# Kernel tuning notes

Measured on AMD Instinct MI355X. Metric: run time of the kernel, lower is better.

The kernel has to match this reference:

```python
import jax, jax.numpy as jnp
import numpy as np
import math

B, CIN, COUT, H, W, K, SDIM = 8, 512, 512, 64, 64, 3, 512
EPS = 1e-8
NEG_SLOPE = 0.2
SCALE = math.sqrt(2.0)


def setup_inputs() -> dict:
    key = jax.random.key(0)
    ks = jax.random.split(key, 7)
    x = jax.random.normal(ks[0], (B, CIN, H, W), jnp.float32)
    style = jax.random.normal(ks[1], (B, SDIM), jnp.float32)
    noise = jax.random.normal(ks[2], (B, 1, H, W), jnp.float32)
    # kernel stored as (kh, kw, Cin, Cout) like keras Conv2D
    fan_in = K * K * CIN
    kernel = jax.random.normal(ks[3], (K, K, CIN, COUT), jnp.float32) / math.sqrt(fan_in)
    style_scale = jax.random.normal(ks[4], (SDIM, COUT), jnp.float32) * 0.02
    bias = jax.random.normal(ks[5], (COUT,), jnp.float32) * 0.01
    noise_weight = jax.random.normal(ks[6], (1,), jnp.float32) * 0.1
    return {"x": x, "style": style, "noise": noise, "kernel": kernel,
            "style_scale": style_scale, "bias": bias, "noise_weight": noise_weight}


def _styled_conv(x, style, noise, kernel, style_scale, bias, noise_weight):
    b = x.shape[0]
    # --- modulation ---
    s = style @ style_scale                              # [B, Cout]
    w = kernel[None] * (s[:, None, None, None, :] + 1.0)  # [B, kh, kw, Cin, Cout]
    # --- demodulation ---
    d = jax.lax.rsqrt(jnp.sum(jnp.square(w), axis=(1, 2, 3)) + EPS)  # [B, Cout]
    w = w * d[:, None, None, None, :]
    # --- per-sample conv via batch-as-groups trick ---
    # weights -> OIHW with O = B*Cout, groups = B
    w_oihw = jnp.transpose(w, (0, 4, 3, 1, 2)).reshape(b * COUT, CIN, K, K)
    x_g = x.reshape(1, b * CIN, H, W)
    out = jax.lax.conv_general_dilated(
        x_g, w_oihw, window_strides=(1, 1), padding="SAME",
        feature_group_count=b,
        dimension_numbers=("NCHW", "OIHW", "NCHW"))
    out = out.reshape(b, COUT, H, W)
    # --- noise injection ---
    out = out + noise_weight[0] * noise                  # noise broadcasts over channels
    # --- fused bias + leaky relu * sqrt(2) ---
    out = jax.nn.leaky_relu(out + bias[None, :, None, None], NEG_SLOPE) * SCALE
    return out


def reference(x, style, noise, kernel, style_scale, bias, noise_weight):
    return _styled_conv(x, style, noise, kernel, style_scale, bias, noise_weight)
```

## Files before the change

kernel.cpp:

```cpp
#include <hip/hip_runtime.h>

#define B_     8
#define CIN_   512
#define COUT_  512
#define HW_    64
#define SDIM_  512
#define NPIX   4096
#define KTOT   4608
#define PADW   66

typedef __attribute__((ext_vector_type(4))) float f32x4;
typedef __attribute__((ext_vector_type(8))) short bf16x8;
typedef __attribute__((ext_vector_type(8))) unsigned short u16x8;

__device__ __forceinline__ float bf2f(unsigned short b) {
    unsigned int u = ((unsigned int)b) << 16;
    return __builtin_bit_cast(float, u);
}
__device__ __forceinline__ unsigned short f2bf(float f) {
    unsigned int u = __builtin_bit_cast(unsigned int, f);
    return (unsigned short)((u + 0x7fffu + ((u >> 16) & 1u)) >> 16);
}
__device__ __forceinline__ float ldin(const void* p, size_t i, int isbf) {
    return isbf ? bf2f(((const unsigned short*)p)[i]) : ((const float*)p)[i];
}

#define GLD16(g, l) __builtin_amdgcn_global_load_lds( \
    (__attribute__((address_space(1))) void*)(g),     \
    (__attribute__((address_space(3))) void*)(l), 16, 0, 0)

__global__ void detect_dtype(const unsigned int* __restrict__ style_u32,
                             int* __restrict__ flag) {
    int t = threadIdx.x;
    unsigned int w = style_u32[t * 4];
    int e = (w >> 7) & 0xFF;
    int isbf = (e >= 110 && e <= 140) ? 1 : 0;
    __shared__ int cnt;
    if (t == 0) cnt = 0;
    __syncthreads();
    atomicAdd(&cnt, isbf);
    __syncthreads();
    if (t == 0) *flag = (cnt >= 128) ? 1 : 0;
}

__global__ void halo_zero(unsigned short* __restrict__ xtp) {
    int idx = blockIdx.x;
    int b = blockIdx.y;
    int y, x;
    if (idx < 66)       { y = 0;  x = idx; }
    else if (idx < 132) { y = 65; x = idx - 66; }
    else if (idx < 196) { x = 0;  y = idx - 131; }
    else                { x = 65; y = idx - 195; }
    unsigned int* dst = (unsigned int*)(xtp + (((size_t)b * PADW + y) * PADW + x) * CIN_);
    dst[threadIdx.x] = 0;
}

__global__ void wt_transpose(const void* __restrict__ kin,
                             unsigned short* __restrict__ wt,
                             const int* __restrict__ flag) {
    __shared__ __align__(16) unsigned short tile[64][72];
    int isbf = *flag;
    int t = threadIdx.x;
    int co0 = blockIdx.x * 64;
    int k0  = blockIdx.y * 64;
    int r = t >> 2, c16 = (t & 3) << 4;
    if (isbf) {
        const unsigned short* src = (const unsigned short*)kin + (size_t)(k0 + r) * COUT_ + co0 + c16;
        *(u16x8*)&tile[r][c16]     = *(const u16x8*)src;
        *(u16x8*)&tile[r][c16 + 8] = *(const u16x8*)(src + 8);
    } else {
        const float* src = (const float*)kin + (size_t)(k0 + r) * COUT_ + co0 + c16;
#pragma unroll
        for (int q = 0; q < 4; ++q) {
            f32x4 v = *(const f32x4*)(src + q * 4);
#pragma unroll
            for (int j = 0; j < 4; ++j) tile[r][c16 + q * 4 + j] = f2bf(v[j]);
        }
    }
    __syncthreads();
    int c = t >> 2, r16 = (t & 3) << 4;
    u16x8 w0, w1;
#pragma unroll
    for (int j = 0; j < 8; ++j) { w0[j] = tile[r16 + j][c]; w1[j] = tile[r16 + 8 + j][c]; }
    unsigned short* dst = wt + (size_t)(co0 + c) * KTOT + k0 + r16;
    *(u16x8*)dst       = w0;
    *(u16x8*)(dst + 8) = w1;
}

__global__ void xpose(const void* __restrict__ x,
                      unsigned short* __restrict__ xtp,
                      const int* __restrict__ flag) {
    __shared__ __align__(16) unsigned short tile[64][72];
    int isbf = *flag;
    int t = threadIdx.x;
    int cit = blockIdx.x;
    int y   = blockIdx.y;
    int b   = blockIdx.z;
    int ci_l = t >> 2, xo = (t & 3) << 4;
    size_t srcoff = (((size_t)(b * CIN_ + cit * 64 + ci_l)) * HW_ + y) * HW_ + xo;
    if (isbf) {
        const unsigned short* src = (const unsigned short*)x + srcoff;
        *(u16x8*)&tile[ci_l][xo]     = *(const u16x8*)src;
        *(u16x8*)&tile[ci_l][xo + 8] = *(const u16x8*)(src + 8);
    } else {
        const float* src = (const float*)x + srcoff;
#pragma unroll
        for (int q = 0; q < 4; ++q) {
            f32x4 v = *(const f32x4*)(src + q * 4);
#pragma unroll
            for (int j = 0; j < 4; ++j) tile[ci_l][xo + q * 4 + j] = f2bf(v[j]);
        }
    }
    __syncthreads();
    int xl = t >> 2, cio = (t & 3) << 4;
    u16x8 w0, w1;
#pragma unroll
    for (int j = 0; j < 8; ++j) { w0[j] = tile[cio + j][xl]; w1[j] = tile[cio + 8 + j][xl]; }
    unsigned short* dst =
        xtp + (((size_t)b * PADW + (y + 1)) * PADW + (xl + 1)) * CIN_ + cit * 64 + cio;
    *(u16x8*)dst       = w0;
    *(u16x8*)(dst + 8) = w1;
}

__global__ void mod_kernel(const void* __restrict__ style,
                           const void* __restrict__ sscale,
                           const unsigned short* __restrict__ wt,
                           float* __restrict__ mmod,
                           const int* __restrict__ flag) {
    int isbf = *flag;
    int co = blockIdx.x, t = threadIdx.x;
    int lane = t & 63, wid = t >> 6;
    float k2 = 0.f;
    const unsigned short* wr = wt + (size_t)co * KTOT;
    for (int k = t; k < KTOT; k += 256) { float v = bf2f(wr[k]); k2 += v * v; }
    float sb[B_];
#pragma unroll
    for (int b = 0; b < B_; ++b) sb[b] = 0.f;
    for (int sd = t; sd < SDIM_; sd += 256) {
        float ss = ldin(sscale, (size_t)sd * COUT_ + co, isbf);
#pragma unroll
        for (int b = 0; b < B_; ++b) sb[b] += ldin(style, b * SDIM_ + sd, isbf) * ss;
    }
    __shared__ float red[4][9];
    float vals[9];
    vals[0] = k2;
#pragma unroll
    for (int b = 0; b < B_; ++b) vals[1 + b] = sb[b];
#pragma unroll
    for (int q = 0; q < 9; ++q) {
        float v = vals[q];
        for (int off = 32; off; off >>= 1) v += __shfl_down(v, off);
        if (lane == 0) red[wid][q] = v;
    }
    __syncthreads();
    if (t < B_) {
        int b = t;
        float k2t = red[0][0] + red[1][0] + red[2][0] + red[3][0];
        float s   = red[0][1 + b] + red[1][1 + b] + red[2][1 + b] + red[3][1 + b];
        float sp1 = s + 1.f;
        mmod[b * COUT_ + co] = sp1 * rsqrtf(sp1 * sp1 * k2t + 1e-8f);
    }
}

__global__ __launch_bounds__(512, 2) void conv_gemm(
    const unsigned short* __restrict__ wt,
    const unsigned short* __restrict__ xtp,
    const float* __restrict__ mmod,
    const void* __restrict__ noise,
    const void* __restrict__ bias,
    const void* __restrict__ nwp,
    void* __restrict__ out,
    const int* __restrict__ flag) {
    __shared__ __align__(1024) unsigned short Asm[2][256 * 64];
    __shared__ __align__(1024) unsigned short Bsm[2][256 * 64];
    int isbf = *flag;
    int tid = threadIdx.x;
    int lane = tid & 63, wid = tid >> 6;
    int lr = lane & 15, hi = lane >> 4;
    int wm = wid >> 2, wn = wid & 3;

    int bid = blockIdx.x;
    int swz = (bid & 7) * 32 + (bid >> 3);
    int gy = swz >> 7;
    int nb = swz & 127;
    int b  = nb >> 4;
    int nt = nb & 15;
    int pl0 = nt << 8;
    int h0  = pl0 >> 6;
    int co0 = gy << 8;

    const unsigned short* xb = xtp + (size_t)b * (PADW * PADW * CIN_);

    f32x4 acc[8][4];
#pragma unroll
    for (int i = 0; i < 8; ++i)
#pragma unroll
        for (int j = 0; j < 4; ++j) acc[i][j] = (f32x4){0.f, 0.f, 0.f, 0.f};

    int rsub = lane >> 3;
    int ce_src = ((lane & 7) ^ rsub) << 3;
    int swzr = (lane & 7) << 3;

    auto stageA = [&](int tt, int pp, int q) {
        const unsigned short* srcA =
            wt + (size_t)(co0 + (q << 6) + (wid << 3) + rsub) * KTOT + (tt << 6) + ce_src;
        GLD16(srcA, (char*)&Asm[pp][0] + (q << 13) + (wid << 10));
    };
    auto stageB = [&](int tt, int pp, int q) {
        int khw = tt >> 3;
        int kh = (khw >= 6) ? 2 : ((khw >= 3) ? 1 : 0);
        int kw = khw - kh * 3;
        int ci0 = (tt & 7) << 6;
        int wc = ((wid << 3) + rsub) & 63;
        const unsigned short* srcB =
            xb + ((size_t)(h0 + q + kh) * PADW + (wc + kw)) * CIN_ + ci0 + ce_src;
        GLD16(srcB, (char*)&Bsm[pp][0] + (q << 13) + (wid << 10));
    };

#pragma unroll
    for (int q = 0; q < 4; ++q) { stageA(0, 0, q); stageB(0, 0, q); }
    asm volatile("s_waitcnt vmcnt(0)" ::: "memory");
    __builtin_amdgcn_s_barrier();
    asm volatile("" ::: "memory");

    for (int t = 0; t < 72; ++t) {
        int p = t & 1, pn = p ^ 1;
        const unsigned short* As = &Asm[p][0];
        const unsigned short* Bs = &Bsm[p][0];

        if (t < 71) {
#pragma unroll
            for (int q = 0; q < 4; ++q) { stageA(t + 1, pn, q); stageB(t + 1, pn, q); }
        }

        bf16x8 a0[4], bk0[4];
#pragma unroll
        for (int i = 0; i < 4; ++i)
            a0[i] = *(const bf16x8*)&As[(((wm << 7) + (i << 4) + lr) << 6) + ((hi << 3) ^ swzr)];
#pragma unroll
        for (int i = 0; i < 4; ++i)
            bk0[i] = *(const bf16x8*)&Bs[(((wn << 6) + (i << 4) + lr) << 6) + ((hi << 3) ^ swzr)];
        __builtin_amdgcn_s_setprio(1);
#pragma unroll
        for (int mf = 0; mf < 4; ++mf)
#pragma unroll
            for (int nf = 0; nf < 4; ++nf)
                acc[mf][nf] = __builtin_amdgcn_mfma_f32_16x16x32_bf16(a0[mf], bk0[nf], acc[mf][nf], 0, 0, 0);
        __builtin_amdgcn_s_setprio(0);

        bf16x8 a1[4];
#pragma unroll
        for (int i = 0; i < 4; ++i)
            a1[i] = *(const bf16x8*)&As[(((wm << 7) + ((i + 4) << 4) + lr) << 6) + ((hi << 3) ^ swzr)];
        __builtin_amdgcn_s_setprio(1);
#pragma unroll
        for (int mf = 0; mf < 4; ++mf)
#pragma unroll
            for (int nf = 0; nf < 4; ++nf)
                acc[mf + 4][nf] = __builtin_amdgcn_mfma_f32_16x16x32_bf16(a1[mf], bk0[nf], acc[mf + 4][nf], 0, 0, 0);
        __builtin_amdgcn_s_setprio(0);

        bf16x8 a2[4], bk1[4];
#pragma unroll
        for (int i = 0; i < 4; ++i)
            a2[i] = *(const bf16x8*)&As[(((wm << 7) + (i << 4) + lr) << 6) + ((32 + (hi << 3)) ^ swzr)];
#pragma unroll
        for (int i = 0; i < 4; ++i)
            bk1[i] = *(const bf16x8*)&Bs[(((wn << 6) + (i << 4) + lr) << 6) + ((32 + (hi << 3)) ^ swzr)];
        __builtin_amdgcn_s_setprio(1);
#pragma unroll
        for (int mf = 0; mf < 4; ++mf)
#pragma unroll
            for (int nf = 0; nf < 4; ++nf)
                acc[mf][nf] = __builtin_amdgcn_mfma_f32_16x16x32_bf16(a2[mf], bk1[nf], acc[mf][nf], 0, 0, 0);
        __builtin_amdgcn_s_setprio(0);

        bf16x8 a3[4];
#pragma unroll
        for (int i = 0; i < 4; ++i)
            a3[i] = *(const bf16x8*)&As[(((wm << 7) + ((i + 4) << 4) + lr) << 6) + ((32 + (hi << 3)) ^ swzr)];
        __builtin_amdgcn_s_setprio(1);
#pragma unroll
        for (int mf = 0; mf < 4; ++mf)
#pragma unroll
            for (int nf = 0; nf < 4; ++nf)
                acc[mf + 4][nf] = __builtin_amdgcn_mfma_f32_16x16x32_bf16(a3[mf], bk1[nf], acc[mf + 4][nf], 0, 0, 0);
        __builtin_amdgcn_s_setprio(0);

        asm volatile("s_waitcnt lgkmcnt(0)" ::: "memory");
        if (t < 71) asm volatile("s_waitcnt vmcnt(0)" ::: "memory");
        __builtin_amdgcn_s_barrier();
        asm volatile("" ::: "memory");
    }

    float nw = ldin(nwp, 0, isbf);
    unsigned short* out16 = (unsigned short*)out;
    float* outf = (float*)out;
#pragma unroll
    for (int mf = 0; mf < 8; ++mf) {
        int cobase = co0 + (wm << 7) + (mf << 4) + (hi << 2);
        f32x4 mv = *(const f32x4*)&mmod[b * COUT_ + cobase];
        float bb[4];
#pragma unroll
        for (int r = 0; r < 4; ++r) bb[r] = ldin(bias, cobase + r, isbf);
#pragma unroll
        for (int nf = 0; nf < 4; ++nf) {
            int pix = pl0 + (wn << 6) + (nf << 4) + lr;
            float nv = nw * ldin(noise, b * NPIX + pix, isbf);
#pragma unroll
            for (int r = 0; r < 4; ++r) {
                float v = acc[mf][nf][r] * mv[r] + nv + bb[r];
                v = (v < 0.f ? v * 0.2f : v) * 1.41421356237f;
                size_t oidx = ((size_t)(b * COUT_ + cobase + r)) * NPIX + pix;
                if (isbf) out16[oidx] = f2bf(v);
                else      outf[oidx]  = v;
            }
        }
    }
}

extern "C" void kernel_launch(void* const* d_in, const int* in_sizes, int n_in,
                              void* d_out, int out_size, void* d_ws, size_t ws_size,
                              hipStream_t stream) {
    const void* x      = d_in[0];
    const void* style  = d_in[1];
    const void* noise  = d_in[2];
    const void* kin    = d_in[3];
    const void* sscale = d_in[4];
    const void* bias   = d_in[5];
    const void* nwp    = d_in[6];

    char* ws = (char*)d_ws;
    int* flag = (int*)ws;
    const size_t xtp_off  = 256;
    const size_t xtp_bytes = (size_t)B_ * PADW * PADW * CIN_ * 2;
    const size_t wt_bytes  = (size_t)COUT_ * KTOT * 2;
    unsigned short* xtp = (unsigned short*)(ws + xtp_off);
    unsigned short* wtr = (unsigned short*)(ws + xtp_off + xtp_bytes);
    float* mmod         = (float*)(ws + xtp_off + xtp_bytes + wt_bytes);

    detect_dtype<<<1, 256, 0, stream>>>((const unsigned int*)style, flag);
    halo_zero<<<dim3(260, 8), 256, 0, stream>>>(xtp);
    wt_transpose<<<dim3(8, 72), 256, 0, stream>>>(kin, wtr, flag);
    xpose<<<dim3(8, 64, 8), 256, 0, stream>>>(x, xtp, flag);
    mod_kernel<<<512, 256, 0, stream>>>(style, sscale, wtr, mmod, flag);
    conv_gemm<<<256, 512, 0, stream>>>(wtr, xtp, mmod, noise, bias, nwp, d_out, flag);
}
```

Measured before the change: 202.8 us.

## Restructure GEMM main loop into 8-phase ping-pong schedule with interleaved staging

Replaces the simple double-buffered K loop, which issued all global-to-LDS loads for the next tile and then waited for all of them, with a two-tile unrolled loop of eight phases. Each phase issues a quarter of the next tile's A/B loads, reads a subset of fragments from LDS, and runs 16 MFMAs under barriers, with partial vmcnt/lgkmcnt waits. The goal is to overlap global loads, LDS reads and MFMA work more finely and keep loads in flight across iterations. In exchange it adds many more barriers per iteration and relies on hand-tuned waitcnt values, which could stall or race if any of those counts are wrong.

```diff
diff --git a/kernel.cpp b/kernel.cpp
--- a/kernel.cpp
+++ b/kernel.cpp
@@ -216,81 +216,155 @@
             xb + ((size_t)(h0 + q + kh) * PADW + (wc + kw)) * CIN_ + ci0 + ce_src;
         GLD16(srcB, (char*)&Bsm[pp][0] + (q << 13) + (wid << 10));
     };
+    auto rdA = [&](const unsigned short* Bp, int mi, int kk) -> bf16x8 {
+        return *(const bf16x8*)&Bp[(((wm << 7) + (mi << 4) + lr) << 6) +
+                                   (((kk << 5) + (hi << 3)) ^ swzr)];
+    };
+    auto rdB = [&](const unsigned short* Bp, int ni, int kk) -> bf16x8 {
+        return *(const bf16x8*)&Bp[(((wn << 6) + (ni << 4) + lr) << 6) +
+                                   (((kk << 5) + (hi << 3)) ^ swzr)];
+    };
+
+#define PH_SYNC12  asm volatile("s_waitcnt lgkmcnt(8)" ::: "memory");
+#define PH_TOP     __builtin_amdgcn_s_barrier(); \
+                   asm volatile("s_waitcnt lgkmcnt(0)" ::: "memory"); \
+                   __builtin_amdgcn_s_setprio(1);
+#define PH_END     __builtin_amdgcn_s_setprio(0);
+#define PH_BAR     __builtin_amdgcn_s_barrier(); asm volatile("" ::: "memory");
 
 #pragma unroll
     for (int q = 0; q < 4; ++q) { stageA(0, 0, q); stageB(0, 0, q); }
-    asm volatile("s_waitcnt vmcnt(0)" ::: "memory");
+    stageB(1, 1, 0); stageB(1, 1, 1); stageA(1, 1, 0); stageA(1, 1, 1);
+    asm volatile("s_waitcnt vmcnt(4)" ::: "memory");
     __builtin_amdgcn_s_barrier();
     asm volatile("" ::: "memory");
 
-    for (int t = 0; t < 72; ++t) {
-        int p = t & 1, pn = p ^ 1;
-        const unsigned short* As = &Asm[p][0];
-        const unsigned short* Bs = &Bsm[p][0];
-
-        if (t < 71) {
-#pragma unroll
-            for (int q = 0; q < 4; ++q) { stageA(t + 1, pn, q); stageB(t + 1, pn, q); }
-        }
-
-        bf16x8 a0[4], bk0[4];
-#pragma unroll
-        for (int i = 0; i < 4; ++i)
-            a0[i] = *(const bf16x8*)&As[(((wm << 7) + (i << 4) + lr) << 6) + ((hi << 3) ^ swzr)];
-#pragma unroll
-        for (int i = 0; i < 4; ++i)
-            bk0[i] = *(const bf16x8*)&Bs[(((wn << 6) + (i << 4) + lr) << 6) + ((hi << 3) ^ swzr)];
-        __builtin_amdgcn_s_setprio(1);
-#pragma unroll
-        for (int mf = 0; mf < 4; ++mf)
-#pragma unroll
-            for (int nf = 0; nf < 4; ++nf)
-                acc[mf][nf] = __builtin_amdgcn_mfma_f32_16x16x32_bf16(a0[mf], bk0[nf], acc[mf][nf], 0, 0, 0);
-        __builtin_amdgcn_s_setprio(0);
-
-        bf16x8 a1[4];
-#pragma unroll
-        for (int i = 0; i < 4; ++i)
-            a1[i] = *(const bf16x8*)&As[(((wm << 7) + ((i + 4) << 4) + lr) << 6) + ((hi << 3) ^ swzr)];
-        __builtin_amdgcn_s_setprio(1);
-#pragma unroll
-        for (int mf = 0; mf < 4; ++mf)
-#pragma unroll
-            for (int nf = 0; nf < 4; ++nf)
-                acc[mf + 4][nf] = __builtin_amdgcn_mfma_f32_16x16x32_bf16(a1[mf], bk0[nf], acc[mf + 4][nf], 0, 0, 0);
-        __builtin_amdgcn_s_setprio(0);
-
-        bf16x8 a2[4], bk1[4];
-#pragma unroll
-        for (int i = 0; i < 4; ++i)
-            a2[i] = *(const bf16x8*)&As[(((wm << 7) + (i << 4) + lr) << 6) + ((32 + (hi << 3)) ^ swzr)];
-#pragma unroll
-        for (int i = 0; i < 4; ++i)
-            bk1[i] = *(const bf16x8*)&Bs[(((wn << 6) + (i << 4) + lr) << 6) + ((32 + (hi << 3)) ^ swzr)];
-        __builtin_amdgcn_s_setprio(1);
-#pragma unroll
-        for (int mf = 0; mf < 4; ++mf)
-#pragma unroll
-            for (int nf = 0; nf < 4; ++nf)
-                acc[mf][nf] = __builtin_amdgcn_mfma_f32_16x16x32_bf16(a2[mf], bk1[nf], acc[mf][nf], 0, 0, 0);
-        __builtin_amdgcn_s_setprio(0);
-
-        bf16x8 a3[4];
-#pragma unroll
-        for (int i = 0; i < 4; ++i)
-            a3[i] = *(const bf16x8*)&As[(((wm << 7) + ((i + 4) << 4) + lr) << 6) + ((32 + (hi << 3)) ^ swzr)];
-        __builtin_amdgcn_s_setprio(1);
-#pragma unroll
-        for (int mf = 0; mf < 4; ++mf)
-#pragma unroll
-            for (int nf = 0; nf < 4; ++nf)
-                acc[mf + 4][nf] = __builtin_amdgcn_mfma_f32_16x16x32_bf16(a3[mf], bk1[nf], acc[mf + 4][nf], 0, 0, 0);
-        __builtin_amdgcn_s_setprio(0);
-
-        asm volatile("s_waitcnt lgkmcnt(0)" ::: "memory");
-        if (t < 71) asm volatile("s_waitcnt vmcnt(0)" ::: "memory");
-        __builtin_amdgcn_s_barrier();
-        asm volatile("" ::: "memory");
+    for (int i = 0; i < 36; ++i) {
+        int tY = 2 * i + 1;
+        bool sg = (i < 35);
+        const unsigned short* Xa = &Asm[0][0];
+        const unsigned short* Xb = &Bsm[0][0];
+        const unsigned short* Ya = &Asm[1][0];
+        const unsigned short* Yb = &Bsm[1][0];
+        bf16x8 aL[4][2], aH[4][2], bL[2][2], bR[2][2];
+
+#pragma unroll
+        for (int mi = 0; mi < 4; ++mi) { aL[mi][0] = rdA(Xa, mi, 0); aL[mi][1] = rdA(Xa, mi, 1); }
+#pragma unroll
+        for (int ni = 0; ni < 2; ++ni) { bL[ni][0] = rdB(Xb, ni, 0); bL[ni][1] = rdB(Xb, ni, 1); }
+        stageA(tY, 1, 2); stageA(tY, 1, 3);
+        PH_SYNC12
+        PH_TOP
+#pragma unroll
+        for (int mi = 0; mi < 4; ++mi)
+#pragma unroll
+            for (int ni = 0; ni < 2; ++ni) {
+                acc[mi][ni] = __builtin_amdgcn_mfma_f32_16x16x32_bf16(aL[mi][0], bL[ni][0], acc[mi][ni], 0, 0, 0);
+                acc[mi][ni] = __builtin_amdgcn_mfma_f32_16x16x32_bf16(aL[mi][1], bL[ni][1], acc[mi][ni], 0, 0, 0);
+            }
+        PH_END
+        PH_BAR
+
+#pragma unroll
+        for (int ni = 0; ni < 2; ++ni) { bR[ni][0] = rdB(Xb, ni + 2, 0); bR[ni][1] = rdB(Xb, ni + 2, 1); }
+        stageB(tY, 1, 2); stageB(tY, 1, 3);
+        PH_TOP
+#pragma unroll
+        for (int mi = 0; mi < 4; ++mi)
+#pragma unroll
+            for (int ni = 0; ni < 2; ++ni) {
+                acc[mi][ni + 2] = __builtin_amdgcn_mfma_f32_16x16x32_bf16(aL[mi][0], bR[ni][0], acc[mi][ni + 2], 0, 0, 0);
+                acc[mi][ni + 2] = __builtin_amdgcn_mfma_f32_16x16x32_bf16(aL[mi][1], bR[ni][1], acc[mi][ni + 2], 0, 0, 0);
+            }
+        PH_END
+        PH_BAR
+
+#pragma unroll
+        for (int mi = 0; mi < 4; ++mi) { aH[mi][0] = rdA(Xa, mi + 4, 0); aH[mi][1] = rdA(Xa, mi + 4, 1); }
+        if (sg) { stageB(2 * i + 2, 0, 0); stageB(2 * i + 2, 0, 1); }
+        PH_TOP
+#pragma unroll
+        for (int mi = 0; mi < 4; ++mi)
+#pragma unroll
+            for (int ni = 0; ni < 2; ++ni) {
+                acc[mi + 4][ni] = __builtin_amdgcn_mfma_f32_16x16x32_bf16(aH[mi][0], bL[ni][0], acc[mi + 4][ni], 0, 0, 0);
+                acc[mi + 4][ni] = __builtin_amdgcn_mfma_f32_16x16x32_bf16(aH[mi][1], bL[ni][1], acc[mi + 4][ni], 0, 0, 0);
+            }
+        PH_END
+        PH_BAR
+
+        if (sg) { stageA(2 * i + 2, 0, 0); stageA(2 * i + 2, 0, 1); }
+        PH_TOP
+#pragma unroll
+        for (int mi = 0; mi < 4; ++mi)
+#pragma unroll
+            for (int ni = 0; ni < 2; ++ni) {
+                acc[mi + 4][ni + 2] = __builtin_amdgcn_mfma_f32_16x16x32_bf16(aH[mi][0], bR[ni][0], acc[mi + 4][ni + 2], 0, 0, 0);
+                acc[mi + 4][ni + 2] = __builtin_amdgcn_mfma_f32_16x16x32_bf16(aH[mi][1], bR[ni][1], acc[mi + 4][ni + 2], 0, 0, 0);
+            }
+        PH_END
+        if (sg) asm volatile("s_waitcnt vmcnt(4)" ::: "memory");
+        else    asm volatile("s_waitcnt vmcnt(0)" ::: "memory");
+        PH_BAR
+
+#pragma unroll
+        for (int mi = 0; mi < 4; ++mi) { aL[mi][0] = rdA(Ya, mi, 0); aL[mi][1] = rdA(Ya, mi, 1); }
+#pragma unroll
+        for (int ni = 0; ni < 2; ++ni) { bL[ni][0] = rdB(Yb, ni, 0); bL[ni][1] = rdB(Yb, ni, 1); }
+        if (sg) { stageB(2 * i + 2, 0, 2); stageB(2 * i + 2, 0, 3); }
+        PH_SYNC12
+        PH_TOP
+#pragma unroll
+        for (int mi = 0; mi < 4; ++mi)
+#pragma unroll
+            for (int ni = 0; ni < 2; ++ni) {
+                acc[mi][ni] = __builtin_amdgcn_mfma_f32_16x16x32_bf16(aL[mi][0], bL[ni][0], acc[mi][ni], 0, 0, 0);
+                acc[mi][ni] = __builtin_amdgcn_mfma_f32_16x16x32_bf16(aL[mi][1], bL[ni][1], acc[mi][ni], 0, 0, 0);
+            }
+        PH_END
+        PH_BAR
+
+#pragma unroll
+        for (int ni = 0; ni < 2; ++ni) { bR[ni][0] = rdB(Yb, ni + 2, 0); bR[ni][1] = rdB(Yb, ni + 2, 1); }
+        if (sg) { stageA(2 * i + 2, 0, 2); stageA(2 * i + 2, 0, 3); }
+        PH_TOP
+#pragma unroll
+        for (int mi = 0; mi < 4; ++mi)
+#pragma unroll
+            for (int ni = 0; ni < 2; ++ni) {
+                acc[mi][ni + 2] = __builtin_amdgcn_mfma_f32_16x16x32_bf16(aL[mi][0], bR[ni][0], acc[mi][ni + 2], 0, 0, 0);
+                acc[mi][ni + 2] = __builtin_amdgcn_mfma_f32_16x16x32_bf16(aL[mi][1], bR[ni][1], acc[mi][ni + 2], 0, 0, 0);
+            }
+        PH_END
+        PH_BAR
+
+#pragma unroll
+        for (int mi = 0; mi < 4; ++mi) { aH[mi][0] = rdA(Ya, mi + 4, 0); aH[mi][1] = rdA(Ya, mi + 4, 1); }
+        if (sg) { stageB(2 * i + 3, 1, 0); stageB(2 * i + 3, 1, 1); }
+        PH_TOP
+#pragma unroll
+        for (int mi = 0; mi < 4; ++mi)
+#pragma unroll
+            for (int ni = 0; ni < 2; ++ni) {
+                acc[mi + 4][ni] = __builtin_amdgcn_mfma_f32_16x16x32_bf16(aH[mi][0], bL[ni][0], acc[mi + 4][ni], 0, 0, 0);
+                acc[mi + 4][ni] = __builtin_amdgcn_mfma_f32_16x16x32_bf16(aH[mi][1], bL[ni][1], acc[mi + 4][ni], 0, 0, 0);
+            }
+        PH_END
+        PH_BAR
+
+        if (sg) { stageA(2 * i + 3, 1, 0); stageA(2 * i + 3, 1, 1); }
+        PH_TOP
+#pragma unroll
+        for (int mi = 0; mi < 4; ++mi)
+#pragma unroll
+            for (int ni = 0; ni < 2; ++ni) {
+                acc[mi + 4][ni + 2] = __builtin_amdgcn_mfma_f32_16x16x32_bf16(aH[mi][0], bR[ni][0], acc[mi + 4][ni + 2], 0, 0, 0);
+                acc[mi + 4][ni + 2] = __builtin_amdgcn_mfma_f32_16x16x32_bf16(aH[mi][1], bR[ni][1], acc[mi + 4][ni + 2], 0, 0, 0);
+            }
+        PH_END
+        if (sg) asm volatile("s_waitcnt vmcnt(4)" ::: "memory");
+        else    asm volatile("s_waitcnt vmcnt(0)" ::: "memory");
+        PH_BAR
     }
 
     float nw = ldin(nwp, 0, isbf);
```

New measurement: 188.2 us. -7.2%, faster.

## Stage input halo window in LDS once per channel tile, reuse across 3x3 taps

Applied to the files above, without the earlier changes.

The padded activation buffer is re-laid out as [b][cin/64][66][66][64] so each 64-channel slab is contiguous. The conv GEMM now loads a 6x72x64 halo window into LDS once per channel tile and reads all nine kernel taps from it with shifted, swizzled offsets, instead of reloading an im2col B tile from global memory at every K step. The K loop order becomes channel-tile outer and tap inner, and the weight staging offsets change to match. The cost is an extra barrier and a non-overlapped window load at each channel-tile boundary, plus possible LDS bank conflicts from the tap-dependent swizzle.

```diff
diff --git a/kernel.cpp b/kernel.cpp
--- a/kernel.cpp
+++ b/kernel.cpp
@@ -43,7 +43,7 @@
     if (t == 0) *flag = (cnt >= 128) ? 1 : 0;
 }
 
-__global__ void halo_zero(unsigned short* __restrict__ xtp) {
+__global__ void halo_zero(unsigned int* __restrict__ xtp2u) {
     int idx = blockIdx.x;
     int b = blockIdx.y;
     int y, x;
@@ -51,8 +51,10 @@
     else if (idx < 132) { y = 65; x = idx - 66; }
     else if (idx < 196) { x = 0;  y = idx - 131; }
     else                { x = 65; y = idx - 195; }
-    unsigned int* dst = (unsigned int*)(xtp + (((size_t)b * PADW + y) * PADW + x) * CIN_);
-    dst[threadIdx.x] = 0;
+    int t = threadIdx.x;
+    int cit = t >> 5, j = t & 31;
+    size_t u32i = ((((size_t)(b * 8 + cit) * 66 + y) * 66 + x) << 5) + j;
+    xtp2u[u32i] = 0;
 }
 
 __global__ void wt_transpose(const void* __restrict__ kin,
@@ -88,7 +90,7 @@
 }
 
 __global__ void xpose(const void* __restrict__ x,
-                      unsigned short* __restrict__ xtp,
+                      unsigned short* __restrict__ xtp2,
                       const int* __restrict__ flag) {
     __shared__ __align__(16) unsigned short tile[64][72];
     int isbf = *flag;
@@ -117,7 +119,7 @@
 #pragma unroll
     for (int j = 0; j < 8; ++j) { w0[j] = tile[cio + j][xl]; w1[j] = tile[cio + 8 + j][xl]; }
     unsigned short* dst =
-        xtp + (((size_t)b * PADW + (y + 1)) * PADW + (xl + 1)) * CIN_ + cit * 64 + cio;
+        xtp2 + ((((size_t)(b * 8 + cit) * 66 + (y + 1)) * 66 + (xl + 1)) << 6) + cio;
     *(u16x8*)dst       = w0;
     *(u16x8*)(dst + 8) = w1;
 }
@@ -164,7 +166,7 @@
 
 __global__ __launch_bounds__(512, 2) void conv_gemm(
     const unsigned short* __restrict__ wt,
-    const unsigned short* __restrict__ xtp,
+    const unsigned short* __restrict__ xtp2,
     const float* __restrict__ mmod,
     const void* __restrict__ noise,
     const void* __restrict__ bias,
@@ -172,7 +174,7 @@
     void* __restrict__ out,
     const int* __restrict__ flag) {
     __shared__ __align__(1024) unsigned short Asm[2][256 * 64];
-    __shared__ __align__(1024) unsigned short Bsm[2][256 * 64];
+    __shared__ __align__(1024) unsigned short Win[6 * 72 * 64];
     int isbf = *flag;
     int tid = threadIdx.x;
     int lane = tid & 63, wid = tid >> 6;
@@ -189,8 +191,6 @@
     int h0  = pl0 >> 6;
     int co0 = gy << 8;
 
-    const unsigned short* xb = xtp + (size_t)b * (PADW * PADW * CIN_);
-
     f32x4 acc[8][4];
 #pragma unroll
     for (int i = 0; i < 8; ++i)
@@ -200,97 +200,117 @@
     int rsub = lane >> 3;
     int ce_src = ((lane & 7) ^ rsub) << 3;
     int swzr = (lane & 7) << 3;
-
-    auto stageA = [&](int tt, int pp, int q) {
+    int wsrc = (rsub << 6) + (((lane & 7) ^ (rsub & 7)) << 3);
+    int l7 = lane & 7;
+    int px[4];
+#pragma unroll
+    for (int ni = 0; ni < 4; ++ni) px[ni] = ((ni << 4) + lr) << 6;
+
+    auto stageA = [&](int koff, int pp, int q) {
         const unsigned short* srcA =
-            wt + (size_t)(co0 + (q << 6) + (wid << 3) + rsub) * KTOT + (tt << 6) + ce_src;
+            wt + (size_t)(co0 + (q << 6) + (wid << 3) + rsub) * KTOT + koff + ce_src;
         GLD16(srcA, (char*)&Asm[pp][0] + (q << 13) + (wid << 10));
     };
-    auto stageB = [&](int tt, int pp, int q) {
-        int khw = tt >> 3;
-        int kh = (khw >= 6) ? 2 : ((khw >= 3) ? 1 : 0);
-        int kw = khw - kh * 3;
-        int ci0 = (tt & 7) << 6;
-        int wc = ((wid << 3) + rsub) & 63;
-        const unsigned short* srcB =
-            xb + ((size_t)(h0 + q + kh) * PADW + (wc + kw)) * CIN_ + ci0 + ce_src;
-        GLD16(srcB, (char*)&Bsm[pp][0] + (q << 13) + (wid << 10));
+    auto stage_win = [&](int cit) {
+        size_t base = ((size_t)(b * 8 + cit) * 66 + h0) * (66 * 64);
+        for (int idx = wid; idx < 54; idx += 8) {
+            int r = idx / 9, g = idx - r * 9;
+            const unsigned short* src = xtp2 + base + (size_t)r * (66 * 64) + (g << 9) + wsrc;
+            GLD16(src, (char*)Win + r * 9216 + (g << 10));
+        }
     };
 
-#pragma unroll
-    for (int q = 0; q < 4; ++q) { stageA(0, 0, q); stageB(0, 0, q); }
+    stage_win(0);
+#pragma unroll
+    for (int q = 0; q < 4; ++q) stageA(0, 0, q);
     asm volatile("s_waitcnt vmcnt(0)" ::: "memory");
     __builtin_amdgcn_s_barrier();
     asm volatile("" ::: "memory");
 
-    for (int t = 0; t < 72; ++t) {
-        int p = t & 1, pn = p ^ 1;
-        const unsigned short* As = &Asm[p][0];
-        const unsigned short* Bs = &Bsm[p][0];
-
-        if (t < 71) {
-#pragma unroll
-            for (int q = 0; q < 4; ++q) { stageA(t + 1, pn, q); stageB(t + 1, pn, q); }
-        }
-
-        bf16x8 a0[4], bk0[4];
-#pragma unroll
-        for (int i = 0; i < 4; ++i)
-            a0[i] = *(const bf16x8*)&As[(((wm << 7) + (i << 4) + lr) << 6) + ((hi << 3) ^ swzr)];
-#pragma unroll
-        for (int i = 0; i < 4; ++i)
-            bk0[i] = *(const bf16x8*)&Bs[(((wn << 6) + (i << 4) + lr) << 6) + ((hi << 3) ^ swzr)];
-        __builtin_amdgcn_s_setprio(1);
-#pragma unroll
-        for (int mf = 0; mf < 4; ++mf)
-#pragma unroll
-            for (int nf = 0; nf < 4; ++nf)
-                acc[mf][nf] = __builtin_amdgcn_mfma_f32_16x16x32_bf16(a0[mf], bk0[nf], acc[mf][nf], 0, 0, 0);
-        __builtin_amdgcn_s_setprio(0);
-
-        bf16x8 a1[4];
-#pragma unroll
-        for (int i = 0; i < 4; ++i)
-            a1[i] = *(const bf16x8*)&As[(((wm << 7) + ((i + 4) << 4) + lr) << 6) + ((hi << 3) ^ swzr)];
-        __builtin_amdgcn_s_setprio(1);
-#pragma unroll
-        for (int mf = 0; mf < 4; ++mf)
-#pragma unroll
-            for (int nf = 0; nf < 4; ++nf)
-                acc[mf + 4][nf] = __builtin_amdgcn_mfma_f32_16x16x32_bf16(a1[mf], bk0[nf], acc[mf + 4][nf], 0, 0, 0);
-        __builtin_amdgcn_s_setprio(0);
-
-        bf16x8 a2[4], bk1[4];
-#pragma unroll
-        for (int i = 0; i < 4; ++i)
-            a2[i] = *(const bf16x8*)&As[(((wm << 7) + (i << 4) + lr) << 6) + ((32 + (hi << 3)) ^ swzr)];
-#pragma unroll
-        for (int i = 0; i < 4; ++i)
-            bk1[i] = *(const bf16x8*)&Bs[(((wn << 6) + (i << 4) + lr) << 6) + ((32 + (hi << 3)) ^ swzr)];
-        __builtin_amdgcn_s_setprio(1);
-#pragma unroll
-        for (int mf = 0; mf < 4; ++mf)
-#pragma unroll
-            for (int nf = 0; nf < 4; ++nf)
-                acc[mf][nf] = __builtin_amdgcn_mfma_f32_16x16x32_bf16(a2[mf], bk1[nf], acc[mf][nf], 0, 0, 0);
-        __builtin_amdgcn_s_setprio(0);
-
-        bf16x8 a3[4];
-#pragma unroll
-        for (int i = 0; i < 4; ++i)
-            a3[i] = *(const bf16x8*)&As[(((wm << 7) + ((i + 4) << 4) + lr) << 6) + ((32 + (hi << 3)) ^ swzr)];
-        __builtin_amdgcn_s_setprio(1);
-#pragma unroll
-        for (int mf = 0; mf < 4; ++mf)
-#pragma unroll
-            for (int nf = 0; nf < 4; ++nf)
-                acc[mf + 4][nf] = __builtin_amdgcn_mfma_f32_16x16x32_bf16(a3[mf], bk1[nf], acc[mf + 4][nf], 0, 0, 0);
-        __builtin_amdgcn_s_setprio(0);
-
-        asm volatile("s_waitcnt lgkmcnt(0)" ::: "memory");
-        if (t < 71) asm volatile("s_waitcnt vmcnt(0)" ::: "memory");
-        __builtin_amdgcn_s_barrier();
-        asm volatile("" ::: "memory");
+    int t = 0;
+    for (int cit = 0; cit < 8; ++cit) {
+        if (cit > 0) {
+            stage_win(cit);
+            asm volatile("s_waitcnt vmcnt(0)" ::: "memory");
+            __builtin_amdgcn_s_barrier();
+            asm volatile("" ::: "memory");
+        }
+        for (int khw = 0; khw < 9; ++khw, ++t) {
+            int p = t & 1, pn = p ^ 1;
+            const unsigned short* As = &Asm[p][0];
+            int kh = (khw >= 6) ? 2 : ((khw >= 3) ? 1 : 0);
+            int kw = khw - kh * 3;
+            int BD = (((wn + kh) * 72) + kw) << 6;
+            int xv = ((l7 + kw) & 7) << 3;
+
+            if (t < 71) {
+                int khw1 = (khw == 8) ? 0 : khw + 1;
+                int cit1 = (khw == 8) ? cit + 1 : cit;
+                int koff1 = khw1 * 512 + (cit1 << 6);
+#pragma unroll
+                for (int q = 0; q < 4; ++q) stageA(koff1, pn, q);
+            }
+
+            bf16x8 a0[4], bk0[4];
+            int kc0 = (hi << 3), kc1 = 32 + (hi << 3);
+#pragma unroll
+            for (int i = 0; i < 4; ++i)
+                a0[i] = *(const bf16x8*)&As[(((wm << 7) + (i << 4) + lr) << 6) + (kc0 ^ swzr)];
+#pragma unroll
+            for (int ni = 0; ni < 4; ++ni)
+                bk0[ni] = *(const bf16x8*)&Win[BD + px[ni] + (kc0 ^ xv)];
+            __builtin_amdgcn_s_setprio(1);
+#pragma unroll
+            for (int mf = 0; mf < 4; ++mf)
+#pragma unroll
+                for (int nf = 0; nf < 4; ++nf)
+                    acc[mf][nf] = __builtin_amdgcn_mfma_f32_16x16x32_bf16(a0[mf], bk0[nf], acc[mf][nf], 0, 0, 0);
+            __builtin_amdgcn_s_setprio(0);
+
+            bf16x8 a1[4];
+#pragma unroll
+            for (int i = 0; i < 4; ++i)
+                a1[i] = *(const bf16x8*)&As[(((wm << 7) + ((i + 4) << 4) + lr) << 6) + (kc0 ^ swzr)];
+            __builtin_amdgcn_s_setprio(1);
+#pragma unroll
+            for (int mf = 0; mf < 4; ++mf)
+#pragma unroll
+                for (int nf = 0; nf < 4; ++nf)
+                    acc[mf + 4][nf] = __builtin_amdgcn_mfma_f32_16x16x32_bf16(a1[mf], bk0[nf], acc[mf + 4][nf], 0, 0, 0);
+            __builtin_amdgcn_s_setprio(0);
+
+            bf16x8 a2[4], bk1[4];
+#pragma unroll
+            for (int i = 0; i < 4; ++i)
+                a2[i] = *(const bf16x8*)&As[(((wm << 7) + (i << 4) + lr) << 6) + (kc1 ^ swzr)];
+#pragma unroll
+            for (int ni = 0; ni < 4; ++ni)
+                bk1[ni] = *(const bf16x8*)&Win[BD + px[ni] + (kc1 ^ xv)];
+            __builtin_amdgcn_s_setprio(1);
+#pragma unroll
+            for (int mf = 0; mf < 4; ++mf)
+#pragma unroll
+                for (int nf = 0; nf < 4; ++nf)
+                    acc[mf][nf] = __builtin_amdgcn_mfma_f32_16x16x32_bf16(a2[mf], bk1[nf], acc[mf][nf], 0, 0, 0);
+            __builtin_amdgcn_s_setprio(0);
+
+            bf16x8 a3[4];
+#pragma unroll
+            for (int i = 0; i < 4; ++i)
+                a3[i] = *(const bf16x8*)&As[(((wm << 7) + ((i + 4) << 4) + lr) << 6) + (kc1 ^ swzr)];
+            __builtin_amdgcn_s_setprio(1);
+#pragma unroll
+            for (int mf = 0; mf < 4; ++mf)
+#pragma unroll
+                for (int nf = 0; nf < 4; ++nf)
+                    acc[mf + 4][nf] = __builtin_amdgcn_mfma_f32_16x16x32_bf16(a3[mf], bk1[nf], acc[mf + 4][nf], 0, 0, 0);
+            __builtin_amdgcn_s_setprio(0);
+
+            asm volatile("s_waitcnt lgkmcnt(0)" ::: "memory");
+            if (t < 71) asm volatile("s_waitcnt vmcnt(0)" ::: "memory");
+            __builtin_amdgcn_s_barrier();
+            asm volatile("" ::: "memory");
+        }
     }
 
     float nw = ldin(nwp, 0, isbf);
@@ -332,17 +352,18 @@
 
     char* ws = (char*)d_ws;
     int* flag = (int*)ws;
-    const size_t xtp_off  = 256;
-    const size_t xtp_bytes = (size_t)B_ * PADW * PADW * CIN_ * 2;
+    const size_t xtp_off   = 256;
+    const size_t xtp_bytes = (size_t)B_ * 8 * 66 * 66 * 64 * 2;
+    const size_t pad       = 4096;
     const size_t wt_bytes  = (size_t)COUT_ * KTOT * 2;
-    unsigned short* xtp = (unsigned short*)(ws + xtp_off);
-    unsigned short* wtr = (unsigned short*)(ws + xtp_off + xtp_bytes);
-    float* mmod         = (float*)(ws + xtp_off + xtp_bytes + wt_bytes);
+    unsigned short* xtp2 = (unsigned short*)(ws + xtp_off);
+    unsigned short* wtr  = (unsigned short*)(ws + xtp_off + xtp_bytes + pad);
+    float* mmod          = (float*)(ws + xtp_off + xtp_bytes + pad + wt_bytes);
 
     detect_dtype<<<1, 256, 0, stream>>>((const unsigned int*)style, flag);
-    halo_zero<<<dim3(260, 8), 256, 0, stream>>>(xtp);
+    halo_zero<<<dim3(260, 8), 256, 0, stream>>>((unsigned int*)xtp2);
     wt_transpose<<<dim3(8, 72), 256, 0, stream>>>(kin, wtr, flag);
-    xpose<<<dim3(8, 64, 8), 256, 0, stream>>>(x, xtp, flag);
+    xpose<<<dim3(8, 64, 8), 256, 0, stream>>>(x, xtp2, flag);
     mod_kernel<<<512, 256, 0, stream>>>(style, sscale, wtr, mmod, flag);
-    conv_gemm<<<256, 512, 0, stream>>>(wtr, xtp, mmod, noise, bias, nwp, d_out, flag);
-}
+    conv_gemm<<<256, 512, 0, stream>>>(wtr, xtp2, mmod, noise, bias, nwp, d_out, flag);
+}
```

Result: faster. 185.8 us (-8.3%).
